# Optimization experiments

Hardware: AMD Instinct MI355X
Metric: run time of the kernel (lower is better)

The kernel has to match this reference:

```python
import jax, jax.numpy as jnp
import numpy as np

B, N, C = 8, 1025, 768  # batch, tokens (1 CLS + 32*32 patches), channels
H = 12                  # heads
D = C // H              # head dim = 64
EPS = 1e-6

def _rot(x):
    # stack([-x[..., 1::2], x[..., ::2]], -1).reshape(x.shape)
    return jnp.stack([-x[..., 1::2], x[..., ::2]], axis=-1).reshape(x.shape)

def apply_rot_embed_cat(x, emb):
    # emb: [N-1, 2*D] = concat(sin, cos); x: [B, H, N-1, D]
    sin, cos = jnp.split(emb, 2, axis=-1)
    return x * cos + _rot(x) * sin

def setup_inputs() -> dict:
    key = jax.random.key(0)
    ks = jax.random.split(key, 8)
    s = 0.02
    return {
        "x": jax.random.normal(ks[0], (B, N, C), jnp.float32),
        "rope": jax.random.normal(ks[1], (N - 1, 2 * D), jnp.float32),
        "w_qkv": jax.random.normal(ks[2], (C, 3 * C), jnp.float32) * s,
        "q_bias": jax.random.normal(ks[3], (C,), jnp.float32) * s,
        "v_bias": jax.random.normal(ks[4], (C,), jnp.float32) * s,
        "gamma": jnp.ones((C,), jnp.float32),
        "beta": jnp.zeros((C,), jnp.float32),
        "w_proj": jax.random.normal(ks[5], (C, C), jnp.float32) * s,
        "b_proj": jnp.zeros((C,), jnp.float32),
    }

def reference(x, rope, w_qkv, q_bias, v_bias, gamma, beta, w_proj, b_proj):
    scale = D ** (-0.5)
    qkv_bias = jnp.concatenate([q_bias, jnp.zeros_like(q_bias), v_bias], axis=0)
    qkv = x @ w_qkv + qkv_bias  # [B, N, 3C]
    qkv = qkv.reshape(B, N, 3, H, D).transpose(2, 0, 3, 1, 4)  # [3, B, H, N, D]
    q, k, v = qkv[0], qkv[1], qkv[2]
    # RoPE on non-CLS tokens only
    q = jnp.concatenate([q[:, :, :1], apply_rot_embed_cat(q[:, :, 1:], rope)], axis=2)
    k = jnp.concatenate([k[:, :, :1], apply_rot_embed_cat(k[:, :, 1:], rope)], axis=2)
    attn = jnp.einsum('bhqd,bhkd->bhqk', q * scale, k)
    attn = jax.nn.softmax(attn, axis=-1)
    y = jnp.einsum('bhqk,bhkd->bhqd', attn, v)
    y = y.transpose(0, 2, 1, 3).reshape(B, N, C)
    # LayerNorm
    mu = jnp.mean(y, axis=-1, keepdims=True)
    var = jnp.mean(jnp.square(y - mu), axis=-1, keepdims=True)
    y = (y - mu) * jax.lax.rsqrt(var + EPS) * gamma + beta
    return y @ w_proj + b_proj
```

## Files before the change

kernel.cpp:

```cpp
#include <hip/hip_runtime.h>

typedef __bf16 bf16_t;
typedef __bf16 bf16x8 __attribute__((ext_vector_type(8)));
typedef float f32x4 __attribute__((ext_vector_type(4)));
typedef float f32x16 __attribute__((ext_vector_type(16)));
typedef unsigned short u16;
typedef unsigned int u32;

#define NTOK 1025
#define MTOT 8200
#define MPAD 8448
#define CDIM 768

__device__ __forceinline__ u16 f2bf(float f) {
  union { float f; unsigned u; } v; v.f = f;
  unsigned r = v.u + 0x7fffu + ((v.u >> 16) & 1u);
  return (u16)(r >> 16);
}
__device__ __forceinline__ float bf2f(u16 h) {
  union { unsigned u; float f; } v; v.u = ((unsigned)h) << 16; return v.f;
}
__device__ __forceinline__ u32 cvtpk(float lo, float hi) {
  u32 r; asm("v_cvt_pk_bf16_f32 %0, %1, %2" : "=v"(r) : "v"(lo), "v"(hi)); return r;
}
__device__ __forceinline__ void gld16(const void* g, void* l) {
  __builtin_amdgcn_global_load_lds(
      (const __attribute__((address_space(1))) unsigned*)g,
      (__attribute__((address_space(3))) unsigned*)l, 16, 0, 0);
}

__global__ void conv_x(const float4* __restrict__ in, u16* __restrict__ out, int n4) {
  int i = blockIdx.x * blockDim.x + threadIdx.x;
  if (i < n4) {
    float4 f = in[i];
    ushort4 o; o.x = f2bf(f.x); o.y = f2bf(f.y); o.z = f2bf(f.z); o.w = f2bf(f.w);
    *(ushort4*)&out[i * 4] = o;
  }
}

__global__ __launch_bounds__(256) void transp(const float* __restrict__ in,
                                              u16* __restrict__ out, int K, int N) {
  __shared__ float tile[32][33];
  int n0 = blockIdx.x * 32, k0 = blockIdx.y * 32;
  int tx = threadIdx.x & 31, ty = threadIdx.x >> 5;
#pragma unroll
  for (int i = 0; i < 4; ++i)
    tile[ty + i * 8][tx] = in[(size_t)(k0 + ty + i * 8) * N + n0 + tx];
  __syncthreads();
#pragma unroll
  for (int i = 0; i < 4; ++i)
    out[(size_t)(n0 + ty + i * 8) * K + k0 + tx] = f2bf(tile[tx][ty + i * 8]);
}

template <bool TRANS>
__device__ __forceinline__ void kloop256(const u16* __restrict__ A, const u16* __restrict__ Bt,
                                         int m0, int n0, u16* As, u16* Bs, int t,
                                         f32x4* acc) {
  const int K = 768;
  int lane = t & 63;
  int ln = lane & 15, hi = lane >> 4;
  int wave = t >> 6;
  int wr = wave >> 1, wc = wave & 1;
  int swz = (ln & 7) << 4;

  for (int k0 = 0; k0 < K; k0 += 64) {
#pragma unroll
    for (int l = 0; l < 4; ++l) {
      int c = t + l * 512;
      int row = c >> 3, cc = c & 7;
      int scol = (cc ^ (row & 7)) * 8;
      gld16(&A[(size_t)(m0 + row) * K + k0 + scol], &As[(size_t)c * 8]);
      gld16(&Bt[(size_t)(n0 + row) * K + k0 + scol], &Bs[(size_t)c * 8]);
    }
    asm volatile("s_waitcnt vmcnt(0)" ::: "memory");
    __builtin_amdgcn_s_barrier();
    asm volatile("" ::: "memory");
#pragma unroll
    for (int kk = 0; kk < 2; ++kk) {
      bf16x8 af[4], bf[8];
#pragma unroll
      for (int i = 0; i < 4; ++i)
        af[i] = *(const bf16x8*)((const char*)&As[(wr * 64 + i * 16 + ln) * 64]
                                 + ((kk * 64 + hi * 16) ^ swz));
#pragma unroll
      for (int j = 0; j < 8; ++j)
        bf[j] = *(const bf16x8*)((const char*)&Bs[(wc * 128 + j * 16 + ln) * 64]
                                 + ((kk * 64 + hi * 16) ^ swz));
      __builtin_amdgcn_s_setprio(1);
      if (TRANS) {
#pragma unroll
        for (int j = 0; j < 8; ++j)
#pragma unroll
          for (int i = 0; i < 4; ++i)
            acc[j * 4 + i] = __builtin_amdgcn_mfma_f32_16x16x32_bf16(bf[j], af[i], acc[j * 4 + i], 0, 0, 0);
      } else {
#pragma unroll
        for (int i = 0; i < 4; ++i)
#pragma unroll
          for (int j = 0; j < 8; ++j)
            acc[i * 8 + j] = __builtin_amdgcn_mfma_f32_16x16x32_bf16(af[i], bf[j], acc[i * 8 + j], 0, 0, 0);
      }
      __builtin_amdgcn_s_setprio(0);
    }
    asm volatile("" ::: "memory");
    __builtin_amdgcn_s_barrier();
  }
}

__global__ __launch_bounds__(512, 2) void qkv_gemm_all(
    const u16* __restrict__ xb, const u16* __restrict__ wqkvt,
    const float* __restrict__ qbias, const float* __restrict__ vbias,
    const float* __restrict__ rope,
    u16* __restrict__ q, u16* __restrict__ kfr, u16* __restrict__ vfr) {
  __shared__ u16 As[256 * 64], Bs[256 * 64];
  const int NBX = 9;
  int tau0 = blockIdx.x;
  int xcd = tau0 & 7, pos = tau0 >> 3;
  int tau = (xcd < 1) ? pos : 38 + (xcd - 1) * 37 + pos;
  int bx = tau % NBX, by = tau / NBX;
  int m0 = by * 256;
  int t = threadIdx.x;
  int lane = t & 63, wave = t >> 6;
  int ln = lane & 15, hi = lane >> 4;
  int wr = wave >> 1, wc = wave & 1;

  f32x4 acc[32] = {};
  int n0 = (bx < 6) ? bx * 256 : 1536 + (bx - 6) * 256;
  if (bx < 6) kloop256<true>(xb, wqkvt, m0, n0, As, Bs, t, acc);
  else        kloop256<false>(xb, wqkvt, m0, n0, As, Bs, t, acc);

  if (bx < 6) {
    const float scale = 0.125f * 1.4426950408889634f;
#pragma unroll
    for (int ii = 0; ii < 4; ++ii) {
      int m = m0 + wr * 64 + ii * 16 + ln;
      if (m < MTOT) {
        int b = m / NTOK;
        int n = m - b * NTOK;
        const float* rp = rope + (size_t)(n - 1) * 128;
#pragma unroll
        for (int jj = 0; jj < 8; ++jj) {
          int c4 = n0 + wc * 128 + jj * 16 + hi * 4;
          int part = (c4 >= CDIM) ? 1 : 0;
          int cc = c4 - part * CDIM;
          int h = cc >> 6, d4 = cc & 63;
          f32x4 a = acc[jj * 4 + ii];
          float v0 = a[0], v1 = a[1], v2 = a[2], v3 = a[3];
          if (part == 0) {
            float4 qb = *(const float4*)(qbias + cc);
            v0 += qb.x; v1 += qb.y; v2 += qb.z; v3 += qb.w;
          }
          float o0, o1, o2, o3;
          if (n > 0) {
            float4 sn = *(const float4*)(rp + d4);
            float4 cs = *(const float4*)(rp + 64 + d4);
            o0 = v0 * cs.x - v1 * sn.x;
            o1 = v1 * cs.y + v0 * sn.y;
            o2 = v2 * cs.z - v3 * sn.z;
            o3 = v3 * cs.w + v2 * sn.w;
          } else { o0 = v0; o1 = v1; o2 = v2; o3 = v3; }
          uint2 w;
          if (part == 0) {
            w.x = cvtpk(o0 * scale, o1 * scale); w.y = cvtpk(o2 * scale, o3 * scale);
            *(uint2*)(q + ((size_t)(h * MPAD + m)) * 64 + d4) = w;
          } else {
            w.x = cvtpk(o0, o1); w.y = cvtpk(o2, o3);
            int kt2 = n >> 5, lqn = n & 31;
            int sF = d4 >> 4, h2d = (d4 >> 3) & 1, j0 = d4 & 7;
            u16* dst = kfr + ((((size_t)(h * 8 + b) * 34 + kt2) * 4 + sF) * 64
                              + h2d * 32 + lqn) * 8 + j0;
            *(uint2*)dst = w;
          }
        }
      }
    }
  } else {
#pragma unroll
    for (int i = 0; i < 4; ++i) {
      int mrow = m0 + wr * 64 + i * 16 + hi * 4;
#pragma unroll
      for (int j = 0; j < 8; ++j) {
        int cv = n0 - 1536 + wc * 128 + j * 16 + ln;
        int h = cv >> 6, d = cv & 63;
        int hf = d >> 5, lqd = d & 31;
        float vb = vbias[cv];
        f32x4 a = acc[i * 8 + j];
#pragma unroll
        for (int r = 0; r < 4; ++r) {
          int mr = mrow + r;
          if (mr < MTOT) {
            int b = mr / NTOK;
            int n = mr - b * NTOK;
            size_t idx = ((((size_t)(h * 8 + b) * 17 + (n >> 6)) * 4 + ((n >> 4) & 3)) * 2 + hf) * 512
                       + (size_t)((((n >> 3) & 1) * 32 + lqd) * 8 + (n & 7));
            vfr[idx] = f2bf(a[r] + vb);
          }
        }
      }
    }
  }
}

template <bool PF, bool MASK>
__device__ __forceinline__ void flash_iter(
    bf16x8 (&kf)[8], bf16x8 (&kn)[8],
    bf16x8 (&vf)[8], bf16x8 (&vn)[8],
    int pftile, int it,
    const u16* kfb, const u16* vfb, int h2,
    const bf16x8 (&qf)[4], f32x16 (&acc)[2], float& l) {
  if (PF) {
    const u16* kp2 = kfb + (size_t)pftile * 4096;
#pragma unroll
    for (int c = 0; c < 2; ++c)
#pragma unroll
      for (int s = 0; s < 4; ++s)
        kn[c * 4 + s] = *(const bf16x8*)(kp2 + c * 2048 + s * 512);
    const u16* vp2 = vfb + (size_t)pftile * 4096;
#pragma unroll
    for (int hf = 0; hf < 2; ++hf)
#pragma unroll
      for (int s = 0; s < 4; ++s)
        vn[hf * 4 + s] = *(const bf16x8*)(vp2 + (s * 2 + hf) * 512);
  }
  f32x16 sc[2] = {};
  __builtin_amdgcn_s_setprio(1);
#pragma unroll
  for (int c = 0; c < 2; ++c)
#pragma unroll
    for (int s = 0; s < 4; ++s)
      sc[c] = __builtin_amdgcn_mfma_f32_32x32x16_bf16(kf[c * 4 + s], qf[s], sc[c], 0, 0, 0);
  __builtin_amdgcn_s_setprio(0);
#pragma unroll
  for (int c = 0; c < 2; ++c)
#pragma unroll
    for (int r = 0; r < 16; ++r)
      sc[c][r] = __builtin_amdgcn_exp2f(sc[c][r]);
  if (MASK) {
#pragma unroll
    for (int c = 0; c < 2; ++c)
#pragma unroll
      for (int r = 0; r < 16; ++r) {
        int kk = it * 64 + c * 32 + (r & 3) + 8 * (r >> 2) + 4 * h2;
        if (kk >= NTOK) sc[c][r] = 0.f;
      }
  }
  float rs = 0.f;
#pragma unroll
  for (int c = 0; c < 2; ++c)
#pragma unroll
    for (int r = 0; r < 16; ++r) rs += sc[c][r];
  l += rs;
  bf16x8 frag[4];
#pragma unroll
  for (int c = 0; c < 2; ++c) {
    u32 k0 = cvtpk(sc[c][0], sc[c][1]),   k1 = cvtpk(sc[c][2], sc[c][3]);
    u32 k2 = cvtpk(sc[c][4], sc[c][5]),   k3 = cvtpk(sc[c][6], sc[c][7]);
    u32 k4 = cvtpk(sc[c][8], sc[c][9]),   k5 = cvtpk(sc[c][10], sc[c][11]);
    u32 k6 = cvtpk(sc[c][12], sc[c][13]), k7 = cvtpk(sc[c][14], sc[c][15]);
    asm("v_permlane32_swap_b32 %0, %1" : "+v"(k0), "+v"(k2));
    asm("v_permlane32_swap_b32 %0, %1" : "+v"(k1), "+v"(k3));
    asm("v_permlane32_swap_b32 %0, %1" : "+v"(k4), "+v"(k6));
    asm("v_permlane32_swap_b32 %0, %1" : "+v"(k5), "+v"(k7));
    union { u32 u[4]; bf16x8 v; } u0, u1;
    u0.u[0] = k0; u0.u[1] = k1; u0.u[2] = k2; u0.u[3] = k3;
    u1.u[0] = k4; u1.u[1] = k5; u1.u[2] = k6; u1.u[3] = k7;
    frag[c * 2] = u0.v; frag[c * 2 + 1] = u1.v;
  }
  __builtin_amdgcn_s_setprio(1);
#pragma unroll
  for (int hf = 0; hf < 2; ++hf)
#pragma unroll
    for (int s = 0; s < 4; ++s)
      acc[hf] = __builtin_amdgcn_mfma_f32_32x32x16_bf16(vf[hf * 4 + s], frag[s], acc[hf], 0, 0, 0);
  __builtin_amdgcn_s_setprio(0);
}

__global__ __launch_bounds__(256, 2) void flash_attn(
    const u16* __restrict__ q, const u16* __restrict__ kfr,
    const u16* __restrict__ vfr, u16* __restrict__ y) {
  int f = blockIdx.x;
  int xcd = f & 7, idx = f >> 3;
  int bh = xcd * 12 + idx / 9;
  int qt = idx - (idx / 9) * 9;
  int b = bh / 12, h = bh - b * 12;
  int t = threadIdx.x, lane = t & 63, w = t >> 6;
  int lq = lane & 31, h2 = lane >> 5;
  int q0 = qt * 128 + w * 32;
  if (q0 >= NTOK) return;
  int qrow = q0 + lq; if (qrow > NTOK - 1) qrow = NTOK - 1;

  const u16* qp = q + ((size_t)(h * MPAD) + (size_t)b * NTOK + qrow) * 64;
  bf16x8 qf[4];
#pragma unroll
  for (int s = 0; s < 4; ++s)
    qf[s] = *(const bf16x8*)&qp[s * 16 + h2 * 8];

  const u16* kfb = kfr + (size_t)(h * 8 + b) * 34 * 2048 + lane * 8;
  const u16* vfb = vfr + (size_t)(h * 8 + b) * 17 * 4096 + lane * 8;

  f32x16 acc[2] = {};
  float l = 0.f;

  bf16x8 ka[8], kb2[8], va[8], vb[8];
#pragma unroll
  for (int c = 0; c < 2; ++c)
#pragma unroll
    for (int s = 0; s < 4; ++s)
      ka[c * 4 + s] = *(const bf16x8*)(kfb + c * 2048 + s * 512);
#pragma unroll
  for (int hf = 0; hf < 2; ++hf)
#pragma unroll
    for (int s = 0; s < 4; ++s)
      va[hf * 4 + s] = *(const bf16x8*)(vfb + (s * 2 + hf) * 512);

#pragma unroll 1
  for (int i2 = 0; i2 < 8; ++i2) {
    flash_iter<true, false>(ka, kb2, va, vb, 2 * i2 + 1, 2 * i2, kfb, vfb, h2, qf, acc, l);
    flash_iter<true, false>(kb2, ka, vb, va, 2 * i2 + 2, 2 * i2 + 1, kfb, vfb, h2, qf, acc, l);
  }
  flash_iter<false, true>(ka, kb2, va, vb, 0, 16, kfb, vfb, h2, qf, acc, l);

  int row = q0 + lq;
  if (row < NTOK) {
    float lt = l + __shfl_xor(l, 32, 64);
    float inv = 1.f / lt;
    u16* yr = y + ((size_t)(b * NTOK + row)) * CDIM + h * 64;
#pragma unroll
    for (int hf = 0; hf < 2; ++hf)
#pragma unroll
      for (int g = 0; g < 4; ++g) {
        int d0 = hf * 32 + 8 * g + 4 * h2;
        ushort4 o;
        o.x = f2bf(acc[hf][g * 4 + 0] * inv);
        o.y = f2bf(acc[hf][g * 4 + 1] * inv);
        o.z = f2bf(acc[hf][g * 4 + 2] * inv);
        o.w = f2bf(acc[hf][g * 4 + 3] * inv);
        *(ushort4*)&yr[d0] = o;
      }
  }
}

__global__ __launch_bounds__(256) void lnorm(const u16* __restrict__ y,
                                             const float* __restrict__ gamma,
                                             const float* __restrict__ beta,
                                             u16* __restrict__ out) {
  int row = blockIdx.x;
  const u16* yr = y + (size_t)row * CDIM;
  int t = threadIdx.x;
  float v[3];
  float s = 0.f, s2 = 0.f;
#pragma unroll
  for (int i = 0; i < 3; ++i) {
    v[i] = bf2f(yr[t + 256 * i]);
    s += v[i]; s2 += v[i] * v[i];
  }
#pragma unroll
  for (int msk = 1; msk < 64; msk <<= 1) {
    s  += __shfl_xor(s, msk, 64);
    s2 += __shfl_xor(s2, msk, 64);
  }
  __shared__ float ws[8];
  int w = t >> 6, lane = t & 63;
  if (lane == 0) { ws[w] = s; ws[4 + w] = s2; }
  __syncthreads();
  s = ws[0] + ws[1] + ws[2] + ws[3];
  s2 = ws[4] + ws[5] + ws[6] + ws[7];
  float mu = s * (1.f / 768.f);
  float var = s2 * (1.f / 768.f) - mu * mu;
  float rstd = rsqrtf(var + 1e-6f);
#pragma unroll
  for (int i = 0; i < 3; ++i) {
    int c = t + 256 * i;
    out[(size_t)row * CDIM + c] = f2bf((v[i] - mu) * rstd * gamma[c] + beta[c]);
  }
}

__global__ __launch_bounds__(512, 2) void proj_gemm(
    const u16* __restrict__ ylb, const u16* __restrict__ wprjt,
    const float* __restrict__ bias, float* __restrict__ out) {
  __shared__ u16 As[256 * 64], Bs[256 * 64];
  const int NBX = 3;
  int tau0 = blockIdx.x;
  int xcd = tau0 & 7, pos = tau0 >> 3;
  int tau = (xcd < 3) ? xcd * 13 + pos : 39 + (xcd - 3) * 12 + pos;
  int bx = tau % NBX, by = tau / NBX;
  int m0 = by * 256, n0 = bx * 256;
  int t = threadIdx.x;
  int lane = t & 63, wave = t >> 6;
  int ln = lane & 15, hi = lane >> 4;
  int wr = wave >> 1, wc = wave & 1;

  f32x4 acc[32] = {};
  kloop256<true>(ylb, wprjt, m0, n0, As, Bs, t, acc);

#pragma unroll
  for (int ii = 0; ii < 4; ++ii) {
    int m = m0 + wr * 64 + ii * 16 + ln;
    if (m < MTOT) {
      float* dr = out + (size_t)m * CDIM;
#pragma unroll
      for (int jj = 0; jj < 8; ++jj) {
        int c4 = n0 + wc * 128 + jj * 16 + hi * 4;
        float4 bv = *(const float4*)(bias + c4);
        f32x4 a = acc[jj * 4 + ii];
        float4 o;
        o.x = a[0] + bv.x;
        o.y = a[1] + bv.y;
        o.z = a[2] + bv.z;
        o.w = a[3] + bv.w;
        *(float4*)(dr + c4) = o;
      }
    }
  }
}

extern "C" void kernel_launch(void* const* d_in, const int* in_sizes, int n_in,
                              void* d_out, int out_size, void* d_ws, size_t ws_size,
                              hipStream_t stream) {
  const float* x      = (const float*)d_in[0];
  const float* rope   = (const float*)d_in[1];
  const float* w_qkv  = (const float*)d_in[2];
  const float* q_bias = (const float*)d_in[3];
  const float* v_bias = (const float*)d_in[4];
  const float* gamma  = (const float*)d_in[5];
  const float* beta   = (const float*)d_in[6];
  const float* w_proj = (const float*)d_in[7];
  const float* b_proj = (const float*)d_in[8];
  float* out = (float*)d_out;

  char* ws = (char*)d_ws;
  u16* xb    = (u16*)(ws);
  u16* ybf   = (u16*)(ws);
  u16* wqkvt = (u16*)(ws + 12976128);
  u16* wprjt = (u16*)(ws + 16515072);
  u16* qbuf  = (u16*)(ws + 17694720);
  u16* ylb   = (u16*)(ws + 17694720);
  u16* kfr   = (u16*)(ws + 30670848);
  u16* vfr   = (u16*)(ws + 44040192);

  conv_x<<<dim3(6150), 256, 0, stream>>>((const float4*)x, xb, 1574400);
  transp<<<dim3(2304 / 32, 768 / 32), 256, 0, stream>>>(w_qkv, wqkvt, 768, 2304);
  transp<<<dim3(768 / 32, 768 / 32), 256, 0, stream>>>(w_proj, wprjt, 768, 768);

  qkv_gemm_all<<<dim3(297), 512, 0, stream>>>(xb, wqkvt, q_bias, v_bias, rope,
                                              qbuf, kfr, vfr);
  flash_attn<<<dim3(864), 256, 0, stream>>>(qbuf, kfr, vfr, ybf);
  lnorm<<<8200, 256, 0, stream>>>(ybf, gamma, beta, ylb);
  proj_gemm<<<dim3(99), 512, 0, stream>>>(ylb, wprjt, b_proj, out);
}
```

Before: 193.8 us.

## Double-buffer LDS tiles in QKV and projection GEMM k-loops

Converts the GEMM k-loop to a two-stage LDS double buffer: the next 64-wide K slab is issued with async global-to-LDS loads while the current slab is consumed by MFMAs, waiting only on the older loads (vmcnt(8)). LDS per block doubles to 128KB, so launch bounds drop from 2 to 1 blocks per CU. This trades occupancy-based latency hiding for explicit intra-block prefetch overlap.

```diff
diff --git a/kernel.cpp b/kernel.cpp
--- a/kernel.cpp
+++ b/kernel.cpp
@@ -53,9 +53,10 @@
 }
 
 template <bool TRANS>
-__device__ __forceinline__ void kloop256(const u16* __restrict__ A, const u16* __restrict__ Bt,
-                                         int m0, int n0, u16* As, u16* Bs, int t,
-                                         f32x4* acc) {
+__device__ __forceinline__ void kloop256db(const u16* __restrict__ A, const u16* __restrict__ Bt,
+                                           int m0, int n0,
+                                           u16 (*As)[16384], u16 (*Bs)[16384],
+                                           int t, f32x4* acc) {
   const int K = 768;
   int lane = t & 63;
   int ln = lane & 15, hi = lane >> 4;
@@ -63,16 +64,26 @@
   int wr = wave >> 1, wc = wave & 1;
   int swz = (ln & 7) << 4;
 
-  for (int k0 = 0; k0 < K; k0 += 64) {
+  auto stage = [&](int buf, int k0) {
 #pragma unroll
     for (int l = 0; l < 4; ++l) {
       int c = t + l * 512;
       int row = c >> 3, cc = c & 7;
       int scol = (cc ^ (row & 7)) * 8;
-      gld16(&A[(size_t)(m0 + row) * K + k0 + scol], &As[(size_t)c * 8]);
-      gld16(&Bt[(size_t)(n0 + row) * K + k0 + scol], &Bs[(size_t)c * 8]);
-    }
-    asm volatile("s_waitcnt vmcnt(0)" ::: "memory");
+      gld16(&A[(size_t)(m0 + row) * K + k0 + scol], &As[buf][(size_t)c * 8]);
+      gld16(&Bt[(size_t)(n0 + row) * K + k0 + scol], &Bs[buf][(size_t)c * 8]);
+    }
+  };
+
+  stage(0, 0);
+  for (int kt = 0; kt < 12; ++kt) {
+    int cur = kt & 1;
+    if (kt < 11) {
+      stage(cur ^ 1, (kt + 1) * 64);
+      asm volatile("s_waitcnt vmcnt(8)" ::: "memory");
+    } else {
+      asm volatile("s_waitcnt vmcnt(0)" ::: "memory");
+    }
     __builtin_amdgcn_s_barrier();
     asm volatile("" ::: "memory");
 #pragma unroll
@@ -80,11 +91,11 @@
       bf16x8 af[4], bf[8];
 #pragma unroll
       for (int i = 0; i < 4; ++i)
-        af[i] = *(const bf16x8*)((const char*)&As[(wr * 64 + i * 16 + ln) * 64]
+        af[i] = *(const bf16x8*)((const char*)&As[cur][(wr * 64 + i * 16 + ln) * 64]
                                  + ((kk * 64 + hi * 16) ^ swz));
 #pragma unroll
       for (int j = 0; j < 8; ++j)
-        bf[j] = *(const bf16x8*)((const char*)&Bs[(wc * 128 + j * 16 + ln) * 64]
+        bf[j] = *(const bf16x8*)((const char*)&Bs[cur][(wc * 128 + j * 16 + ln) * 64]
                                  + ((kk * 64 + hi * 16) ^ swz));
       __builtin_amdgcn_s_setprio(1);
       if (TRANS) {
@@ -107,12 +118,12 @@
   }
 }
 
-__global__ __launch_bounds__(512, 2) void qkv_gemm_all(
+__global__ __launch_bounds__(512, 1) void qkv_gemm_all(
     const u16* __restrict__ xb, const u16* __restrict__ wqkvt,
     const float* __restrict__ qbias, const float* __restrict__ vbias,
     const float* __restrict__ rope,
     u16* __restrict__ q, u16* __restrict__ kfr, u16* __restrict__ vfr) {
-  __shared__ u16 As[256 * 64], Bs[256 * 64];
+  __shared__ u16 As[2][16384], Bs[2][16384];
   const int NBX = 9;
   int tau0 = blockIdx.x;
   int xcd = tau0 & 7, pos = tau0 >> 3;
@@ -126,8 +137,8 @@
 
   f32x4 acc[32] = {};
   int n0 = (bx < 6) ? bx * 256 : 1536 + (bx - 6) * 256;
-  if (bx < 6) kloop256<true>(xb, wqkvt, m0, n0, As, Bs, t, acc);
-  else        kloop256<false>(xb, wqkvt, m0, n0, As, Bs, t, acc);
+  if (bx < 6) kloop256db<true>(xb, wqkvt, m0, n0, As, Bs, t, acc);
+  else        kloop256db<false>(xb, wqkvt, m0, n0, As, Bs, t, acc);
 
   if (bx < 6) {
     const float scale = 0.125f * 1.4426950408889634f;
@@ -375,10 +386,10 @@
   }
 }
 
-__global__ __launch_bounds__(512, 2) void proj_gemm(
+__global__ __launch_bounds__(512, 1) void proj_gemm(
     const u16* __restrict__ ylb, const u16* __restrict__ wprjt,
     const float* __restrict__ bias, float* __restrict__ out) {
-  __shared__ u16 As[256 * 64], Bs[256 * 64];
+  __shared__ u16 As[2][16384], Bs[2][16384];
   const int NBX = 3;
   int tau0 = blockIdx.x;
   int xcd = tau0 & 7, pos = tau0 >> 3;
@@ -391,7 +402,7 @@
   int wr = wave >> 1, wc = wave & 1;
 
   f32x4 acc[32] = {};
-  kloop256<true>(ylb, wprjt, m0, n0, As, Bs, t, acc);
+  kloop256db<true>(ylb, wprjt, m0, n0, As, Bs, t, acc);
 
 #pragma unroll
   for (int ii = 0; ii < 4; ++ii) {
```

New measurement: 186.3 us. 3.9% less time.
